# Kernel optimization log

Hardware: AMD Instinct MI355X
Metric: run time of the kernel (lower is better)

Reference implementation:

```python
import jax, jax.numpy as jnp
import numpy as np
import math

B, S, D_VEC, D_HEAD = 4, 4096, 1024, 256


def setup_inputs() -> dict:
    key = jax.random.key(0)
    ks = jax.random.split(key, 10)
    scale = 0.02
    return {
        "x_q": jax.random.normal(ks[0], (B, S, D_VEC), dtype=jnp.float32),
        "x_k": jax.random.normal(ks[1], (B, S, D_VEC), dtype=jnp.float32),
        "x_v": jax.random.normal(ks[2], (B, S, D_VEC), dtype=jnp.float32),
        "mask": jax.random.randint(ks[3], (B, S, S), 0, 2, dtype=jnp.int32),
        "wq_w": jax.random.normal(ks[4], (D_HEAD, D_VEC), dtype=jnp.float32) * scale,
        "wq_b": jnp.zeros((D_HEAD,), dtype=jnp.float32),
        "wk_w": jax.random.normal(ks[5], (D_HEAD, D_VEC), dtype=jnp.float32) * scale,
        "wk_b": jnp.zeros((D_HEAD,), dtype=jnp.float32),
        "wv_w": jax.random.normal(ks[6], (D_HEAD, D_VEC), dtype=jnp.float32) * scale,
        "wv_b": jnp.zeros((D_HEAD,), dtype=jnp.float32),
    }


def reference(x_q, x_k, x_v, mask, wq_w, wq_b, wk_w, wk_b, wv_w, wv_b):
    # Linear projections (torch nn.Linear: x @ W^T + b)
    q = jnp.einsum("bsd,hd->bsh", x_q, wq_w) + wq_b  # [B,S,H]
    k = jnp.einsum("bsd,hd->bsh", x_k, wk_w) + wk_b
    v = jnp.einsum("bsd,hd->bsh", x_v, wv_w) + wv_b
    scores = jnp.einsum("bqh,bkh->bqk", q, k) / math.sqrt(D_HEAD)  # [B,Sq,Sk]
    # NOTE: original uses masked_fill(mask==0, 0) BEFORE softmax (fills with 0, not -inf)
    scores = jnp.where(mask == 0, jnp.zeros((), dtype=scores.dtype), scores)
    attn = jax.nn.softmax(scores, axis=-1)
    return jnp.einsum("bqk,bkh->bqh", attn, v)  # [B,S,H]
```

## Files before the change

kernel.cpp:

```cpp
#include <hip/hip_runtime.h>
#include <cstdint>
#include <cstddef>

#define S_LEN 4096
#define DVEC  1024
#define DH    256

typedef __attribute__((ext_vector_type(8))) short short8;
typedef __attribute__((ext_vector_type(4))) float f32x4;
typedef __attribute__((ext_vector_type(4))) unsigned short ushort4v;

__device__ __forceinline__ unsigned short f2bf(float f) {
  unsigned u = __builtin_bit_cast(unsigned, f);
  u += 0x7FFFu + ((u >> 16) & 1u);
  return (unsigned short)(u >> 16);
}

__device__ __forceinline__ void gl2lds16(const void* g, void* lds) {
  __builtin_amdgcn_global_load_lds(
      (const __attribute__((address_space(1))) unsigned int*)g,
      (__attribute__((address_space(3))) unsigned int*)lds, 16, 0, 0);
}

__global__ void wcvt_kernel(const float* __restrict__ wq,
                            const float* __restrict__ wk,
                            const float* __restrict__ wv,
                            unsigned short* __restrict__ wbf) {
  int t   = blockIdx.x * 256 + threadIdx.x;
  int idx = t * 4;
  int m   = idx >> 18;
  int off = idx & 262143;
  const float* src = (m == 0) ? wq : (m == 1) ? wk : wv;
  float scale = (m == 0) ? 0.0625f : 1.0f;
  f32x4 v = *(const f32x4*)(src + off);
  ushort4v o;
  o.x = f2bf(v.x * scale);
  o.y = f2bf(v.y * scale);
  o.z = f2bf(v.z * scale);
  o.w = f2bf(v.w * scale);
  *(ushort4v*)(wbf + idx) = o;
}

__global__ void proj_kernel(const float* __restrict__ xq,
                            const float* __restrict__ xk,
                            const float* __restrict__ xv,
                            const unsigned short* __restrict__ wbf,
                            const float* __restrict__ bq,
                            const float* __restrict__ bk,
                            const float* __restrict__ bv,
                            unsigned short* __restrict__ qbf,
                            unsigned short* __restrict__ kbf,
                            unsigned short* __restrict__ vtbf) {
  const int tid  = threadIdx.x;
  const int lane = tid & 63;
  const int w    = tid >> 6;
  const int z    = blockIdx.z;
  const int m0   = blockIdx.x * 64;

  const float* x = (z == 0) ? xq : (z == 1) ? xk : xv;
  const unsigned short* wz = wbf + (size_t)z * (DH * DVEC);
  const float* bias = (z == 0) ? bq : (z == 1) ? bk : bv;
  const float bscale = (z == 0) ? 0.0625f : 1.0f;

  __shared__ float At[2][64 * 32];

  f32x4 zero = {0.f, 0.f, 0.f, 0.f};
  f32x4 acc[4][4];
#pragma unroll
  for (int i = 0; i < 4; ++i)
#pragma unroll
    for (int j = 0; j < 4; ++j) acc[i][j] = zero;

  auto stage = [&](int kt, int buf) {
    char* dstb = (char*)&At[buf][0] + w * 2048;
#pragma unroll
    for (int i = 0; i < 2; ++i) {
      int lin  = w * 2048 + i * 1024 + lane * 16;
      int row  = lin >> 7;
      int scol = (lin ^ ((row & 7) << 4)) & 127;
      gl2lds16((const char*)x + ((size_t)(m0 + row) * DVEC + kt * 32) * 4 + scol,
               dstb + i * 1024);
    }
  };

  stage(0, 0);
  __syncthreads();

  for (int kt = 0; kt < 32; ++kt) {
    const int buf = kt & 1;
    if (kt + 1 < 32) stage(kt + 1, buf ^ 1);

    short8 bfr[4];
#pragma unroll
    for (int cf = 0; cf < 4; ++cf) {
      int h = w * 64 + cf * 16 + (lane & 15);
      int d = kt * 32 + (lane >> 4) * 8;
      bfr[cf] = *(const short8*)(wz + (size_t)h * DVEC + d);
    }
    const char* ab = (const char*)&At[buf][0];
#pragma unroll
    for (int rf = 0; rf < 4; ++rf) {
      int row = rf * 16 + (lane & 15);
      int c0  = row * 128 + (lane >> 4) * 32;
      int sw  = (row & 7) << 4;
      f32x4 v0 = *(const f32x4*)(ab + (c0 ^ sw));
      f32x4 v1 = *(const f32x4*)(ab + ((c0 + 16) ^ sw));
      short8 af;
      af[0] = (short)f2bf(v0.x); af[1] = (short)f2bf(v0.y);
      af[2] = (short)f2bf(v0.z); af[3] = (short)f2bf(v0.w);
      af[4] = (short)f2bf(v1.x); af[5] = (short)f2bf(v1.y);
      af[6] = (short)f2bf(v1.z); af[7] = (short)f2bf(v1.w);
#pragma unroll
      for (int cf = 0; cf < 4; ++cf)
        acc[rf][cf] = __builtin_amdgcn_mfma_f32_16x16x32_bf16(af, bfr[cf], acc[rf][cf], 0, 0, 0);
    }
    __syncthreads();
  }

  float bvv[4];
#pragma unroll
  for (int cf = 0; cf < 4; ++cf)
    bvv[cf] = bias[w * 64 + cf * 16 + (lane & 15)] * bscale;

  if (z < 2) {
    unsigned short* o = (z == 0) ? qbf : kbf;
#pragma unroll
    for (int rf = 0; rf < 4; ++rf)
#pragma unroll
      for (int cf = 0; cf < 4; ++cf)
#pragma unroll
        for (int r = 0; r < 4; ++r) {
          int m = m0 + rf * 16 + (lane >> 4) * 4 + r;
          int h = w * 64 + cf * 16 + (lane & 15);
          o[(size_t)m * DH + h] = f2bf(acc[rf][cf][r] + bvv[cf]);
        }
  } else {
    int bb = m0 >> 12;
    int sl = m0 & 4095;
#pragma unroll
    for (int rf = 0; rf < 4; ++rf)
#pragma unroll
      for (int cf = 0; cf < 4; ++cf) {
        int s = sl + rf * 16 + (lane >> 4) * 4;
        int h = w * 64 + cf * 16 + (lane & 15);
        ushort4v o;
        o.x = f2bf(acc[rf][cf][0] + bvv[cf]);
        o.y = f2bf(acc[rf][cf][1] + bvv[cf]);
        o.z = f2bf(acc[rf][cf][2] + bvv[cf]);
        o.w = f2bf(acc[rf][cf][3] + bvv[cf]);
        *(ushort4v*)(vtbf + ((size_t)(bb * DH + h)) * S_LEN + s) = o;
      }
  }
}

__global__ void __launch_bounds__(512, 2)
attn_kernel(const unsigned short* __restrict__ qbf,
            const unsigned short* __restrict__ kbf,
            const unsigned short* __restrict__ vtbf,
            const int* __restrict__ mask,
            float* __restrict__ out) {
  const int tid  = threadIdx.x;
  const int lane = tid & 63;
  const int w    = tid >> 6;
  const int j    = lane & 15;
  const int g    = lane >> 4;

  const int kvs = w & 3;
  const int qh  = w >> 2;
  const int qs  = w >> 2;
  const int hs  = w & 3;

  const int bx = blockIdx.x;
  const int x  = bx & 7;
  const int b  = x >> 1;
  const int qt = (bx >> 3) * 2 + (x & 1);
  const int m0 = qt * 64;

  __shared__ char sbuf[140288];

  short8 qreg[2][8];
#pragma unroll
  for (int qf = 0; qf < 2; ++qf) {
    const unsigned short* qrow =
        qbf + ((size_t)(b * S_LEN + m0 + qh * 32 + qf * 16 + j)) * DH + g * 8;
#pragma unroll
    for (int kc = 0; kc < 8; ++kc) qreg[qf][kc] = *(const short8*)(qrow + kc * 32);
  }

  f32x4 zero = {0.f, 0.f, 0.f, 0.f};
  f32x4 acc[2][4];
#pragma unroll
  for (int a = 0; a < 2; ++a)
#pragma unroll
    for (int hf = 0; hf < 4; ++hf) acc[a][hf] = zero;
  float lrow[2][4] = {{0.f, 0.f, 0.f, 0.f}, {0.f, 0.f, 0.f, 0.f}};

  const int* mb = mask + ((size_t)(b * S_LEN + m0 + qh * 32 + g * 4)) * S_LEN + kvs * 16 + j;

  auto stageK = [&](int t, int buf) {
    const char* src = (const char*)kbf + ((size_t)(b * S_LEN) + t * 64) * 512;
    char* dst = sbuf + buf * 32768 + w * 4096;
#pragma unroll
    for (int i = 0; i < 4; ++i) {
      int rid = w * 4 + i;
      int ks  = rid >> 3;
      int kc  = rid & 7;
      gl2lds16(src + (size_t)(ks * 16 + j) * 512 + kc * 64 + g * 16, dst + i * 1024);
    }
  };
  auto stageV = [&](int t, int buf) {
    char* dst = sbuf + 65536 + buf * 32768 + w * 4096;
#pragma unroll
    for (int i = 0; i < 4; ++i) {
      int rid = w * 4 + i;
      int h16 = rid >> 1;
      int kc2 = rid & 1;
      const char* src = (const char*)vtbf +
          (((size_t)(b * DH + h16 * 16 + j)) * S_LEN + t * 64 + kc2 * 32 + g * 8) * 2;
      gl2lds16(src, dst + i * 1024);
    }
  };

  int mcur[8], mnext[8];
#pragma unroll
  for (int qf = 0; qf < 2; ++qf)
#pragma unroll
    for (int r = 0; r < 4; ++r) mcur[qf * 4 + r] = mb[(qf * 16 + r) * S_LEN];
  stageK(0, 0);
  stageV(0, 0);
  __syncthreads();

  const int pwbase = 131072 + (kvs >> 1) * 1024 + ((kvs & 1) * 2 + (j >> 3)) * 256 + (j & 7) * 2;

  const int NT = S_LEN / 64;
  for (int t = 0; t < NT; ++t) {
    const int buf = t & 1;
    if (t + 1 < NT) {
#pragma unroll
      for (int qf = 0; qf < 2; ++qf)
#pragma unroll
        for (int r = 0; r < 4; ++r)
          mnext[qf * 4 + r] = mb[(qf * 16 + r) * S_LEN + (t + 1) * 64];
      stageK(t + 1, buf ^ 1);
    }

    const char* kb = sbuf + buf * 32768 + kvs * 8192;
    f32x4 s0[2], s1[2];
    s0[0] = zero; s0[1] = zero; s1[0] = zero; s1[1] = zero;
    __builtin_amdgcn_s_setprio(1);
#pragma unroll
    for (int kc = 0; kc < 8; kc += 2) {
      short8 k0 = *(const short8*)(kb + kc * 1024 + lane * 16);
      short8 k1 = *(const short8*)(kb + (kc + 1) * 1024 + lane * 16);
      s0[0] = __builtin_amdgcn_mfma_f32_16x16x32_bf16(qreg[0][kc], k0, s0[0], 0, 0, 0);
      s0[1] = __builtin_amdgcn_mfma_f32_16x16x32_bf16(qreg[1][kc], k0, s0[1], 0, 0, 0);
      s1[0] = __builtin_amdgcn_mfma_f32_16x16x32_bf16(qreg[0][kc + 1], k1, s1[0], 0, 0, 0);
      s1[1] = __builtin_amdgcn_mfma_f32_16x16x32_bf16(qreg[1][kc + 1], k1, s1[1], 0, 0, 0);
    }
    __builtin_amdgcn_s_setprio(0);

#pragma unroll
    for (int qf = 0; qf < 2; ++qf) {
      int cb = pwbase + (qh * 2 + qf) * 2048;
#pragma unroll
      for (int r = 0; r < 4; ++r) {
        float sv = s0[qf][r] + s1[qf][r];
        sv = mcur[qf * 4 + r] ? sv : 0.0f;
        float e = __expf(sv);
        lrow[qf][r] += e;
        *(unsigned short*)(sbuf + cb + (r * 4 + g) * 16) = f2bf(e);
      }
    }
    __syncthreads();

    if (t + 1 < NT) stageV(t + 1, buf ^ 1);

    const char* vb = sbuf + 65536 + buf * 32768 + hs * 8192;
    short8 pf[2][2];
#pragma unroll
    for (int qf2 = 0; qf2 < 2; ++qf2)
#pragma unroll
      for (int kc2 = 0; kc2 < 2; ++kc2)
        pf[qf2][kc2] = *(const short8*)(sbuf + 131072 + ((qs * 2 + qf2) * 2 + kc2) * 1024 + lane * 16);
    __builtin_amdgcn_s_setprio(1);
#pragma unroll
    for (int hf = 0; hf < 4; ++hf) {
      short8 v0 = *(const short8*)(vb + (hf * 2 + 0) * 1024 + lane * 16);
      short8 v1 = *(const short8*)(vb + (hf * 2 + 1) * 1024 + lane * 16);
      acc[0][hf] = __builtin_amdgcn_mfma_f32_16x16x32_bf16(pf[0][0], v0, acc[0][hf], 0, 0, 0);
      acc[1][hf] = __builtin_amdgcn_mfma_f32_16x16x32_bf16(pf[1][0], v0, acc[1][hf], 0, 0, 0);
      acc[0][hf] = __builtin_amdgcn_mfma_f32_16x16x32_bf16(pf[0][1], v1, acc[0][hf], 0, 0, 0);
      acc[1][hf] = __builtin_amdgcn_mfma_f32_16x16x32_bf16(pf[1][1], v1, acc[1][hf], 0, 0, 0);
    }
    __builtin_amdgcn_s_setprio(0);

#pragma unroll
    for (int i = 0; i < 8; ++i) mcur[i] = mnext[i];
    __syncthreads();
  }

#pragma unroll
  for (int qf = 0; qf < 2; ++qf)
#pragma unroll
    for (int r = 0; r < 4; ++r) {
#pragma unroll
      for (int off = 1; off < 16; off <<= 1)
        lrow[qf][r] += __shfl_xor(lrow[qf][r], off, 64);
    }
  float* lbuf = (float*)(sbuf + 139264);
  if (j == 0) {
#pragma unroll
    for (int qf = 0; qf < 2; ++qf)
#pragma unroll
      for (int r = 0; r < 4; ++r)
        lbuf[(qh * 32 + qf * 16 + g * 4 + r) * 4 + kvs] = lrow[qf][r];
  }
  __syncthreads();

#pragma unroll
  for (int qf2 = 0; qf2 < 2; ++qf2)
#pragma unroll
    for (int rr = 0; rr < 4; ++rr) {
      int qb = qs * 32 + qf2 * 16 + rr * 4 + g;
      f32x4 lv = *(const f32x4*)&lbuf[qb * 4];
      float linv = 1.0f / (lv[0] + lv[1] + lv[2] + lv[3]);
      float* orow = out + ((size_t)(b * S_LEN + m0 + qb)) * DH + hs * 64 + j;
#pragma unroll
      for (int hf = 0; hf < 4; ++hf)
        orow[hf * 16] = acc[qf2][hf][rr] * linv;
    }
}

extern "C" void kernel_launch(void* const* d_in, const int* in_sizes, int n_in,
                              void* d_out, int out_size, void* d_ws, size_t ws_size,
                              hipStream_t stream) {
  const float* xq = (const float*)d_in[0];
  const float* xk = (const float*)d_in[1];
  const float* xv = (const float*)d_in[2];
  const int* mask = (const int*)d_in[3];
  const float* wq = (const float*)d_in[4];
  const float* bq = (const float*)d_in[5];
  const float* wk = (const float*)d_in[6];
  const float* bk = (const float*)d_in[7];
  const float* wv = (const float*)d_in[8];
  const float* bv = (const float*)d_in[9];
  float* out = (float*)d_out;

  char* ws = (char*)d_ws;
  unsigned short* wbf  = (unsigned short*)(ws);
  unsigned short* qbf  = (unsigned short*)(ws + (2ull  << 20));
  unsigned short* kbf  = (unsigned short*)(ws + (10ull << 20));
  unsigned short* vtbf = (unsigned short*)(ws + (18ull << 20));

  hipLaunchKernelGGL(wcvt_kernel, dim3(768), dim3(256), 0, stream, wq, wk, wv, wbf);
  hipLaunchKernelGGL(proj_kernel, dim3(256, 1, 3), dim3(256), 0, stream,
                     xq, xk, xv, wbf, bq, bk, bv, qbf, kbf, vtbf);
  hipLaunchKernelGGL(attn_kernel, dim3(256), dim3(512), 0, stream,
                     qbf, kbf, vtbf, mask, out);
}
```

Baseline: 275.3 us.

## Warp-specialize attention: split QK/softmax and PV waves, halve query tile

Restructures the attention kernel so waves 0-3 compute QK^T, masking and exp for a 32-row query tile while waves 4-7 run the PV matmul for the previous KV tile, forming a one-stage software pipeline. V is read straight from global memory instead of being staged through LDS, which cuts LDS use and doubles the grid with a higher occupancy target. The aim is to overlap the softmax/exp phase with the PV MFMAs and raise occupancy. In exchange the K tile is loaded per 32 query rows instead of 64, doubling K traffic, and the V reads from global may expose latency.

```diff
diff --git a/kernel.cpp b/kernel.cpp
--- a/kernel.cpp
+++ b/kernel.cpp
@@ -153,7 +153,7 @@
   }
 }
 
-__global__ void __launch_bounds__(512, 2)
+__global__ void __launch_bounds__(512, 4)
 attn_kernel(const unsigned short* __restrict__ qbf,
             const unsigned short* __restrict__ kbf,
             const unsigned short* __restrict__ vtbf,
@@ -165,41 +165,52 @@
   const int j    = lane & 15;
   const int g    = lane >> 4;
 
-  const int kvs = w & 3;
-  const int qh  = w >> 2;
-  const int qs  = w >> 2;
-  const int hs  = w & 3;
-
   const int bx = blockIdx.x;
   const int x  = bx & 7;
   const int b  = x >> 1;
   const int qt = (bx >> 3) * 2 + (x & 1);
-  const int m0 = qt * 64;
-
-  __shared__ char sbuf[140288];
-
+  const int m0 = qt * 32;
+
+  __shared__ char sbuf[74240];
+  float* lbuf = (float*)(sbuf + 73728);
+
+  const int NT = S_LEN / 64;
+
+  f32x4 zero = {0.f, 0.f, 0.f, 0.f};
+
+  const int kvs = w;
   short8 qreg[2][8];
-#pragma unroll
-  for (int qf = 0; qf < 2; ++qf) {
-    const unsigned short* qrow =
-        qbf + ((size_t)(b * S_LEN + m0 + qh * 32 + qf * 16 + j)) * DH + g * 8;
-#pragma unroll
-    for (int kc = 0; kc < 8; ++kc) qreg[qf][kc] = *(const short8*)(qrow + kc * 32);
-  }
-
-  f32x4 zero = {0.f, 0.f, 0.f, 0.f};
+  float lrow[2][4] = {{0.f,0.f,0.f,0.f},{0.f,0.f,0.f,0.f}};
+  int mcur[8], mnext[8];
+  const int* mb = nullptr;
+  int pjoff = 0;
+  if (w < 4) {
+#pragma unroll
+    for (int qf = 0; qf < 2; ++qf) {
+      const unsigned short* qrow =
+          qbf + ((size_t)(b * S_LEN + m0 + qf * 16 + j)) * DH + g * 8;
+#pragma unroll
+      for (int kc = 0; kc < 8; ++kc) qreg[qf][kc] = *(const short8*)(qrow + kc * 32);
+    }
+    mb = mask + ((size_t)(b * S_LEN + m0 + g * 4)) * S_LEN + kvs * 16 + j;
+    int jj = (kvs & 1) * 16 + j;
+    pjoff = (jj >> 3) * 16 + (jj & 7) * 2;
+#pragma unroll
+    for (int qf = 0; qf < 2; ++qf)
+#pragma unroll
+      for (int r = 0; r < 4; ++r) mcur[qf * 4 + r] = mb[(qf * 16 + r) * S_LEN];
+  }
+
+  const int hs = w - 4;
   f32x4 acc[2][4];
 #pragma unroll
   for (int a = 0; a < 2; ++a)
 #pragma unroll
     for (int hf = 0; hf < 4; ++hf) acc[a][hf] = zero;
-  float lrow[2][4] = {{0.f, 0.f, 0.f, 0.f}, {0.f, 0.f, 0.f, 0.f}};
-
-  const int* mb = mask + ((size_t)(b * S_LEN + m0 + qh * 32 + g * 4)) * S_LEN + kvs * 16 + j;
-
-  auto stageK = [&](int t, int buf) {
-    const char* src = (const char*)kbf + ((size_t)(b * S_LEN) + t * 64) * 512;
-    char* dst = sbuf + buf * 32768 + w * 4096;
+
+  auto stageK = [&](int t1) {
+    const char* src = (const char*)kbf + ((size_t)(b * S_LEN + t1 * 64)) * 512;
+    char* dst = sbuf + (t1 & 1) * 32768 + w * 4096;
 #pragma unroll
     for (int i = 0; i < 4; ++i) {
       int rid = w * 4 + i;
@@ -208,127 +219,112 @@
       gl2lds16(src + (size_t)(ks * 16 + j) * 512 + kc * 64 + g * 16, dst + i * 1024);
     }
   };
-  auto stageV = [&](int t, int buf) {
-    char* dst = sbuf + 65536 + buf * 32768 + w * 4096;
-#pragma unroll
-    for (int i = 0; i < 4; ++i) {
-      int rid = w * 4 + i;
-      int h16 = rid >> 1;
-      int kc2 = rid & 1;
-      const char* src = (const char*)vtbf +
-          (((size_t)(b * DH + h16 * 16 + j)) * S_LEN + t * 64 + kc2 * 32 + g * 8) * 2;
-      gl2lds16(src, dst + i * 1024);
-    }
-  };
-
-  int mcur[8], mnext[8];
-#pragma unroll
-  for (int qf = 0; qf < 2; ++qf)
-#pragma unroll
-    for (int r = 0; r < 4; ++r) mcur[qf * 4 + r] = mb[(qf * 16 + r) * S_LEN];
-  stageK(0, 0);
-  stageV(0, 0);
-  __syncthreads();
-
-  const int pwbase = 131072 + (kvs >> 1) * 1024 + ((kvs & 1) * 2 + (j >> 3)) * 256 + (j & 7) * 2;
-
-  const int NT = S_LEN / 64;
-  for (int t = 0; t < NT; ++t) {
-    const int buf = t & 1;
-    if (t + 1 < NT) {
-#pragma unroll
-      for (int qf = 0; qf < 2; ++qf)
-#pragma unroll
-        for (int r = 0; r < 4; ++r)
-          mnext[qf * 4 + r] = mb[(qf * 16 + r) * S_LEN + (t + 1) * 64];
-      stageK(t + 1, buf ^ 1);
-    }
-
-    const char* kb = sbuf + buf * 32768 + kvs * 8192;
-    f32x4 s0[2], s1[2];
-    s0[0] = zero; s0[1] = zero; s1[0] = zero; s1[1] = zero;
+
+  auto pv = [&](int u) {
+    const char* pb = sbuf + 65536 + (u & 1) * 4096;
+    short8 pf[2][2];
+#pragma unroll
+    for (int qf2 = 0; qf2 < 2; ++qf2)
+#pragma unroll
+      for (int kvc = 0; kvc < 2; ++kvc)
+        pf[qf2][kvc] = *(const short8*)(pb + (qf2 * 2 + kvc) * 1024 + j * 64 + g * 16);
+    const unsigned short* vb =
+        vtbf + ((size_t)(b * DH + hs * 64 + j)) * S_LEN + u * 64 + g * 8;
     __builtin_amdgcn_s_setprio(1);
 #pragma unroll
-    for (int kc = 0; kc < 8; kc += 2) {
-      short8 k0 = *(const short8*)(kb + kc * 1024 + lane * 16);
-      short8 k1 = *(const short8*)(kb + (kc + 1) * 1024 + lane * 16);
-      s0[0] = __builtin_amdgcn_mfma_f32_16x16x32_bf16(qreg[0][kc], k0, s0[0], 0, 0, 0);
-      s0[1] = __builtin_amdgcn_mfma_f32_16x16x32_bf16(qreg[1][kc], k0, s0[1], 0, 0, 0);
-      s1[0] = __builtin_amdgcn_mfma_f32_16x16x32_bf16(qreg[0][kc + 1], k1, s1[0], 0, 0, 0);
-      s1[1] = __builtin_amdgcn_mfma_f32_16x16x32_bf16(qreg[1][kc + 1], k1, s1[1], 0, 0, 0);
-    }
-    __builtin_amdgcn_s_setprio(0);
-
-#pragma unroll
-    for (int qf = 0; qf < 2; ++qf) {
-      int cb = pwbase + (qh * 2 + qf) * 2048;
-#pragma unroll
-      for (int r = 0; r < 4; ++r) {
-        float sv = s0[qf][r] + s1[qf][r];
-        sv = mcur[qf * 4 + r] ? sv : 0.0f;
-        float e = __expf(sv);
-        lrow[qf][r] += e;
-        *(unsigned short*)(sbuf + cb + (r * 4 + g) * 16) = f2bf(e);
-      }
-    }
-    __syncthreads();
-
-    if (t + 1 < NT) stageV(t + 1, buf ^ 1);
-
-    const char* vb = sbuf + 65536 + buf * 32768 + hs * 8192;
-    short8 pf[2][2];
-#pragma unroll
-    for (int qf2 = 0; qf2 < 2; ++qf2)
-#pragma unroll
-      for (int kc2 = 0; kc2 < 2; ++kc2)
-        pf[qf2][kc2] = *(const short8*)(sbuf + 131072 + ((qs * 2 + qf2) * 2 + kc2) * 1024 + lane * 16);
-    __builtin_amdgcn_s_setprio(1);
-#pragma unroll
     for (int hf = 0; hf < 4; ++hf) {
-      short8 v0 = *(const short8*)(vb + (hf * 2 + 0) * 1024 + lane * 16);
-      short8 v1 = *(const short8*)(vb + (hf * 2 + 1) * 1024 + lane * 16);
+      short8 v0 = *(const short8*)(vb + (size_t)(hf * 16) * S_LEN);
+      short8 v1 = *(const short8*)(vb + (size_t)(hf * 16) * S_LEN + 32);
       acc[0][hf] = __builtin_amdgcn_mfma_f32_16x16x32_bf16(pf[0][0], v0, acc[0][hf], 0, 0, 0);
       acc[1][hf] = __builtin_amdgcn_mfma_f32_16x16x32_bf16(pf[1][0], v0, acc[1][hf], 0, 0, 0);
       acc[0][hf] = __builtin_amdgcn_mfma_f32_16x16x32_bf16(pf[0][1], v1, acc[0][hf], 0, 0, 0);
       acc[1][hf] = __builtin_amdgcn_mfma_f32_16x16x32_bf16(pf[1][1], v1, acc[1][hf], 0, 0, 0);
     }
     __builtin_amdgcn_s_setprio(0);
-
-#pragma unroll
-    for (int i = 0; i < 8; ++i) mcur[i] = mnext[i];
+  };
+
+  stageK(0);
+  __syncthreads();
+
+  for (int t = 0; t < NT; ++t) {
+    if (t + 1 < NT) stageK(t + 1);
+
+    if (w < 4) {
+      const char* kb = sbuf + (t & 1) * 32768;
+      f32x4 s0 = zero, s1 = zero;
+      __builtin_amdgcn_s_setprio(1);
+#pragma unroll
+      for (int kc = 0; kc < 8; ++kc) {
+        short8 kf = *(const short8*)(kb + (kvs * 8 + kc) * 1024 + lane * 16);
+        s0 = __builtin_amdgcn_mfma_f32_16x16x32_bf16(qreg[0][kc], kf, s0, 0, 0, 0);
+        s1 = __builtin_amdgcn_mfma_f32_16x16x32_bf16(qreg[1][kc], kf, s1, 0, 0, 0);
+      }
+      __builtin_amdgcn_s_setprio(0);
+
+      if (t + 1 < NT) {
+#pragma unroll
+        for (int qf = 0; qf < 2; ++qf)
+#pragma unroll
+          for (int r = 0; r < 4; ++r)
+            mnext[qf * 4 + r] = mb[(qf * 16 + r) * S_LEN + (t + 1) * 64];
+      }
+
+      char* pb = sbuf + 65536 + (t & 1) * 4096;
+#pragma unroll
+      for (int qf = 0; qf < 2; ++qf) {
+        int sbase = (qf * 2 + (kvs >> 1)) * 1024 + pjoff;
+#pragma unroll
+        for (int r = 0; r < 4; ++r) {
+          float sv = qf ? s1[r] : s0[r];
+          sv = mcur[qf * 4 + r] ? sv : 0.0f;
+          float e = __expf(sv);
+          lrow[qf][r] += e;
+          *(unsigned short*)(pb + sbase + (g * 4 + r) * 64) = f2bf(e);
+        }
+      }
+#pragma unroll
+      for (int i = 0; i < 8; ++i) mcur[i] = mnext[i];
+    } else {
+      if (t > 0) pv(t - 1);
+    }
+
     __syncthreads();
   }
 
-#pragma unroll
-  for (int qf = 0; qf < 2; ++qf)
-#pragma unroll
-    for (int r = 0; r < 4; ++r) {
-#pragma unroll
-      for (int off = 1; off < 16; off <<= 1)
-        lrow[qf][r] += __shfl_xor(lrow[qf][r], off, 64);
-    }
-  float* lbuf = (float*)(sbuf + 139264);
-  if (j == 0) {
+  if (w >= 4) {
+    pv(NT - 1);
+  } else {
 #pragma unroll
     for (int qf = 0; qf < 2; ++qf)
 #pragma unroll
-      for (int r = 0; r < 4; ++r)
-        lbuf[(qh * 32 + qf * 16 + g * 4 + r) * 4 + kvs] = lrow[qf][r];
+      for (int r = 0; r < 4; ++r) {
+#pragma unroll
+        for (int off = 1; off < 16; off <<= 1)
+          lrow[qf][r] += __shfl_xor(lrow[qf][r], off, 64);
+      }
+    if (j == 0) {
+#pragma unroll
+      for (int qf = 0; qf < 2; ++qf)
+#pragma unroll
+        for (int r = 0; r < 4; ++r)
+          lbuf[(qf * 16 + g * 4 + r) * 4 + kvs] = lrow[qf][r];
+    }
   }
   __syncthreads();
 
-#pragma unroll
-  for (int qf2 = 0; qf2 < 2; ++qf2)
-#pragma unroll
-    for (int rr = 0; rr < 4; ++rr) {
-      int qb = qs * 32 + qf2 * 16 + rr * 4 + g;
-      f32x4 lv = *(const f32x4*)&lbuf[qb * 4];
-      float linv = 1.0f / (lv[0] + lv[1] + lv[2] + lv[3]);
-      float* orow = out + ((size_t)(b * S_LEN + m0 + qb)) * DH + hs * 64 + j;
-#pragma unroll
-      for (int hf = 0; hf < 4; ++hf)
-        orow[hf * 16] = acc[qf2][hf][rr] * linv;
-    }
+  if (w >= 4) {
+#pragma unroll
+    for (int qf2 = 0; qf2 < 2; ++qf2)
+#pragma unroll
+      for (int r = 0; r < 4; ++r) {
+        f32x4 lv = *(const f32x4*)&lbuf[(qf2 * 16 + g * 4 + r) * 4];
+        float linv = 1.0f / (lv[0] + lv[1] + lv[2] + lv[3]);
+        float* orow = out + ((size_t)(b * S_LEN + m0 + qf2 * 16 + g * 4 + r)) * DH + hs * 64 + j;
+#pragma unroll
+        for (int hf = 0; hf < 4; ++hf)
+          orow[hf * 16] = acc[qf2][hf][r] * linv;
+      }
+  }
 }
 
 extern "C" void kernel_launch(void* const* d_in, const int* in_sizes, int n_in,
@@ -355,6 +351,6 @@
   hipLaunchKernelGGL(wcvt_kernel, dim3(768), dim3(256), 0, stream, wq, wk, wv, wbf);
   hipLaunchKernelGGL(proj_kernel, dim3(256, 1, 3), dim3(256), 0, stream,
                      xq, xk, xv, wbf, bq, bk, bv, qbf, kbf, vtbf);
-  hipLaunchKernelGGL(attn_kernel, dim3(256), dim3(512), 0, stream,
+  hipLaunchKernelGGL(attn_kernel, dim3(512), dim3(512), 0, stream,
                      qbf, kbf, vtbf, mask, out);
 }
```

New measurement: 442.7 us. 60.8% more time.

## Pack mask into bitmask, load V directly to registers, shrink LDS

Applied to the files above, without the earlier changes.

Adds a pre-pass kernel that compresses the int32 mask into 64-bit ballot words, so the attention kernel reads one bit per element instead of a 4-byte int per score. V tiles are now loaded straight from global memory into registers instead of being staged through LDS. This halves the shared-memory footprint and raises the launch bound to 4 waves-per-EU hint. The cost is an extra full pass over the 256MB mask, plus uncoalesced-ish direct V loads. The attention grid of 256 blocks still gives at most one block per CU, so the extra occupancy may go unused.

```diff
diff --git a/kernel.cpp b/kernel.cpp
--- a/kernel.cpp
+++ b/kernel.cpp
@@ -9,6 +9,7 @@
 typedef __attribute__((ext_vector_type(8))) short short8;
 typedef __attribute__((ext_vector_type(4))) float f32x4;
 typedef __attribute__((ext_vector_type(4))) unsigned short ushort4v;
+typedef unsigned long long ull;
 
 __device__ __forceinline__ unsigned short f2bf(float f) {
   unsigned u = __builtin_bit_cast(unsigned, f);
@@ -20,6 +21,31 @@
   __builtin_amdgcn_global_load_lds(
       (const __attribute__((address_space(1))) unsigned int*)g,
       (__attribute__((address_space(3))) unsigned int*)lds, 16, 0, 0);
+}
+
+__global__ void mcomp_kernel(const int* __restrict__ mask,
+                             ull* __restrict__ mbits) {
+  const int lane = threadIdx.x & 63;
+  const int wid  = (int)((blockIdx.x * blockDim.x + threadIdx.x) >> 6);
+  const size_t base = (size_t)wid * 256;
+#pragma unroll 4
+  for (int i = 0; i < 64; ++i) {
+    size_t w0 = base + (size_t)i * 4;
+    int v0 = mask[(w0 + 0) * 64 + lane];
+    int v1 = mask[(w0 + 1) * 64 + lane];
+    int v2 = mask[(w0 + 2) * 64 + lane];
+    int v3 = mask[(w0 + 3) * 64 + lane];
+    ull b0 = __ballot(v0 != 0);
+    ull b1 = __ballot(v1 != 0);
+    ull b2 = __ballot(v2 != 0);
+    ull b3 = __ballot(v3 != 0);
+    if (lane == 0) {
+      mbits[w0 + 0] = b0;
+      mbits[w0 + 1] = b1;
+      mbits[w0 + 2] = b2;
+      mbits[w0 + 3] = b3;
+    }
+  }
 }
 
 __global__ void wcvt_kernel(const float* __restrict__ wq,
@@ -153,11 +179,11 @@
   }
 }
 
-__global__ void __launch_bounds__(512, 2)
+__global__ void __launch_bounds__(512, 4)
 attn_kernel(const unsigned short* __restrict__ qbf,
             const unsigned short* __restrict__ kbf,
             const unsigned short* __restrict__ vtbf,
-            const int* __restrict__ mask,
+            const ull* __restrict__ mbits,
             float* __restrict__ out) {
   const int tid  = threadIdx.x;
   const int lane = tid & 63;
@@ -176,7 +202,8 @@
   const int qt = (bx >> 3) * 2 + (x & 1);
   const int m0 = qt * 64;
 
-  __shared__ char sbuf[140288];
+  __shared__ char sbuf[74752];
+  float* lbuf = (float*)(sbuf + 73728);
 
   short8 qreg[2][8];
 #pragma unroll
@@ -193,13 +220,16 @@
   for (int a = 0; a < 2; ++a)
 #pragma unroll
     for (int hf = 0; hf < 4; ++hf) acc[a][hf] = zero;
-  float lrow[2][4] = {{0.f, 0.f, 0.f, 0.f}, {0.f, 0.f, 0.f, 0.f}};
-
-  const int* mb = mask + ((size_t)(b * S_LEN + m0 + qh * 32 + g * 4)) * S_LEN + kvs * 16 + j;
-
-  auto stageK = [&](int t, int buf) {
-    const char* src = (const char*)kbf + ((size_t)(b * S_LEN) + t * 64) * 512;
-    char* dst = sbuf + buf * 32768 + w * 4096;
+  float lrow[2][4] = {{0.f,0.f,0.f,0.f},{0.f,0.f,0.f,0.f}};
+  short8 vreg[4][2];
+
+  const ull* mwb = mbits + ((size_t)(b * S_LEN + m0 + qh * 32 + g * 4)) * 64;
+  const int mbit = kvs * 16 + j;
+  int mcur[8], mnext[8];
+
+  auto stageK = [&](int t1, int bufbase) {
+    const char* src = (const char*)kbf + ((size_t)(b * S_LEN + t1 * 64)) * 512;
+    char* dst = sbuf + bufbase + w * 4096;
 #pragma unroll
     for (int i = 0; i < 4; ++i) {
       int rid = w * 4 + i;
@@ -208,40 +238,39 @@
       gl2lds16(src + (size_t)(ks * 16 + j) * 512 + kc * 64 + g * 16, dst + i * 1024);
     }
   };
-  auto stageV = [&](int t, int buf) {
-    char* dst = sbuf + 65536 + buf * 32768 + w * 4096;
-#pragma unroll
-    for (int i = 0; i < 4; ++i) {
-      int rid = w * 4 + i;
-      int h16 = rid >> 1;
-      int kc2 = rid & 1;
-      const char* src = (const char*)vtbf +
-          (((size_t)(b * DH + h16 * 16 + j)) * S_LEN + t * 64 + kc2 * 32 + g * 8) * 2;
-      gl2lds16(src, dst + i * 1024);
-    }
-  };
-
-  int mcur[8], mnext[8];
+
+  const unsigned short* vbase =
+      vtbf + ((size_t)(b * DH + hs * 64 + j)) * S_LEN;
+
+  const int pwbase = 65536 + (kvs >> 1) * 1024 + ((kvs & 1) * 2 + (j >> 3)) * 256 + (j & 7) * 2;
+
+  stageK(0, 0);
 #pragma unroll
   for (int qf = 0; qf < 2; ++qf)
 #pragma unroll
-    for (int r = 0; r < 4; ++r) mcur[qf * 4 + r] = mb[(qf * 16 + r) * S_LEN];
-  stageK(0, 0);
-  stageV(0, 0);
+    for (int r = 0; r < 4; ++r)
+      mcur[qf * 4 + r] = (int)((mwb[(qf * 16 + r) * 64] >> mbit) & 1ull);
   __syncthreads();
-
-  const int pwbase = 131072 + (kvs >> 1) * 1024 + ((kvs & 1) * 2 + (j >> 3)) * 256 + (j & 7) * 2;
 
   const int NT = S_LEN / 64;
   for (int t = 0; t < NT; ++t) {
     const int buf = t & 1;
     if (t + 1 < NT) {
+      stageK(t + 1, (buf ^ 1) * 32768);
 #pragma unroll
       for (int qf = 0; qf < 2; ++qf)
 #pragma unroll
         for (int r = 0; r < 4; ++r)
-          mnext[qf * 4 + r] = mb[(qf * 16 + r) * S_LEN + (t + 1) * 64];
-      stageK(t + 1, buf ^ 1);
+          mnext[qf * 4 + r] = (int)((mwb[(qf * 16 + r) * 64 + t + 1] >> mbit) & 1ull);
+    }
+
+    {
+      const unsigned short* vt = vbase + t * 64 + g * 8;
+#pragma unroll
+      for (int hf = 0; hf < 4; ++hf)
+#pragma unroll
+        for (int kvc = 0; kvc < 2; ++kvc)
+          vreg[hf][kvc] = *(const short8*)(vt + (size_t)(hf * 16) * S_LEN + kvc * 32);
     }
 
     const char* kb = sbuf + buf * 32768 + kvs * 8192;
@@ -273,24 +302,19 @@
     }
     __syncthreads();
 
-    if (t + 1 < NT) stageV(t + 1, buf ^ 1);
-
-    const char* vb = sbuf + 65536 + buf * 32768 + hs * 8192;
     short8 pf[2][2];
 #pragma unroll
     for (int qf2 = 0; qf2 < 2; ++qf2)
 #pragma unroll
-      for (int kc2 = 0; kc2 < 2; ++kc2)
-        pf[qf2][kc2] = *(const short8*)(sbuf + 131072 + ((qs * 2 + qf2) * 2 + kc2) * 1024 + lane * 16);
+      for (int kvc = 0; kvc < 2; ++kvc)
+        pf[qf2][kvc] = *(const short8*)(sbuf + 65536 + ((qs * 2 + qf2) * 2 + kvc) * 1024 + lane * 16);
     __builtin_amdgcn_s_setprio(1);
 #pragma unroll
     for (int hf = 0; hf < 4; ++hf) {
-      short8 v0 = *(const short8*)(vb + (hf * 2 + 0) * 1024 + lane * 16);
-      short8 v1 = *(const short8*)(vb + (hf * 2 + 1) * 1024 + lane * 16);
-      acc[0][hf] = __builtin_amdgcn_mfma_f32_16x16x32_bf16(pf[0][0], v0, acc[0][hf], 0, 0, 0);
-      acc[1][hf] = __builtin_amdgcn_mfma_f32_16x16x32_bf16(pf[1][0], v0, acc[1][hf], 0, 0, 0);
-      acc[0][hf] = __builtin_amdgcn_mfma_f32_16x16x32_bf16(pf[0][1], v1, acc[0][hf], 0, 0, 0);
-      acc[1][hf] = __builtin_amdgcn_mfma_f32_16x16x32_bf16(pf[1][1], v1, acc[1][hf], 0, 0, 0);
+      acc[0][hf] = __builtin_amdgcn_mfma_f32_16x16x32_bf16(pf[0][0], vreg[hf][0], acc[0][hf], 0, 0, 0);
+      acc[1][hf] = __builtin_amdgcn_mfma_f32_16x16x32_bf16(pf[1][0], vreg[hf][0], acc[1][hf], 0, 0, 0);
+      acc[0][hf] = __builtin_amdgcn_mfma_f32_16x16x32_bf16(pf[0][1], vreg[hf][1], acc[0][hf], 0, 0, 0);
+      acc[1][hf] = __builtin_amdgcn_mfma_f32_16x16x32_bf16(pf[1][1], vreg[hf][1], acc[1][hf], 0, 0, 0);
     }
     __builtin_amdgcn_s_setprio(0);
 
@@ -307,7 +331,6 @@
       for (int off = 1; off < 16; off <<= 1)
         lrow[qf][r] += __shfl_xor(lrow[qf][r], off, 64);
     }
-  float* lbuf = (float*)(sbuf + 139264);
   if (j == 0) {
 #pragma unroll
     for (int qf = 0; qf < 2; ++qf)
@@ -351,10 +374,12 @@
   unsigned short* qbf  = (unsigned short*)(ws + (2ull  << 20));
   unsigned short* kbf  = (unsigned short*)(ws + (10ull << 20));
   unsigned short* vtbf = (unsigned short*)(ws + (18ull << 20));
-
+  ull*            mbit = (ull*)           (ws + (26ull << 20));
+
+  hipLaunchKernelGGL(mcomp_kernel, dim3(1024), dim3(256), 0, stream, mask, mbit);
   hipLaunchKernelGGL(wcvt_kernel, dim3(768), dim3(256), 0, stream, wq, wk, wv, wbf);
   hipLaunchKernelGGL(proj_kernel, dim3(256, 1, 3), dim3(256), 0, stream,
                      xq, xk, xv, wbf, bq, bk, bv, qbf, kbf, vtbf);
   hipLaunchKernelGGL(attn_kernel, dim3(256), dim3(512), 0, stream,
-                     qbf, kbf, vtbf, mask, out);
-}
+                     qbf, kbf, vtbf, mbit, out);
+}
```

New measurement: 763.1 us. 2.77x slower.

## Precompress int32 mask into bitmasks with ballot before attention

Applied to the files above, without the earlier changes.

Adds a pre-pass kernel that reads the int32 mask with coalesced loads and packs each 64-key chunk into a 64-bit word using wave ballots. The attention kernel then reads one 64-bit word per row per tile and extracts its bit, instead of issuing scattered 4-byte mask loads inside the main loop. This aims to take mask bandwidth and latency off the attention kernel's critical loop. The cost is an extra launch that still streams the full mask once, plus a small bitmask write and read. The pre-pass keeps only a few loads in flight per wave, so it could limit how fully memory bandwidth is used.

```diff
diff --git a/kernel.cpp b/kernel.cpp
--- a/kernel.cpp
+++ b/kernel.cpp
@@ -9,6 +9,7 @@
 typedef __attribute__((ext_vector_type(8))) short short8;
 typedef __attribute__((ext_vector_type(4))) float f32x4;
 typedef __attribute__((ext_vector_type(4))) unsigned short ushort4v;
+typedef unsigned long long ull;
 
 __device__ __forceinline__ unsigned short f2bf(float f) {
   unsigned u = __builtin_bit_cast(unsigned, f);
@@ -20,6 +21,31 @@
   __builtin_amdgcn_global_load_lds(
       (const __attribute__((address_space(1))) unsigned int*)g,
       (__attribute__((address_space(3))) unsigned int*)lds, 16, 0, 0);
+}
+
+__global__ void mcomp_kernel(const int* __restrict__ mask,
+                             ull* __restrict__ mbits) {
+  const int lane = threadIdx.x & 63;
+  const int wid  = (int)((blockIdx.x * blockDim.x + threadIdx.x) >> 6);
+  const size_t base = (size_t)wid * 256;
+#pragma unroll 4
+  for (int i = 0; i < 64; ++i) {
+    size_t w0 = base + (size_t)i * 4;
+    int v0 = mask[(w0 + 0) * 64 + lane];
+    int v1 = mask[(w0 + 1) * 64 + lane];
+    int v2 = mask[(w0 + 2) * 64 + lane];
+    int v3 = mask[(w0 + 3) * 64 + lane];
+    ull b0 = __ballot(v0 != 0);
+    ull b1 = __ballot(v1 != 0);
+    ull b2 = __ballot(v2 != 0);
+    ull b3 = __ballot(v3 != 0);
+    if (lane == 0) {
+      mbits[w0 + 0] = b0;
+      mbits[w0 + 1] = b1;
+      mbits[w0 + 2] = b2;
+      mbits[w0 + 3] = b3;
+    }
+  }
 }
 
 __global__ void wcvt_kernel(const float* __restrict__ wq,
@@ -157,7 +183,7 @@
 attn_kernel(const unsigned short* __restrict__ qbf,
             const unsigned short* __restrict__ kbf,
             const unsigned short* __restrict__ vtbf,
-            const int* __restrict__ mask,
+            const ull* __restrict__ mbits,
             float* __restrict__ out) {
   const int tid  = threadIdx.x;
   const int lane = tid & 63;
@@ -195,7 +221,8 @@
     for (int hf = 0; hf < 4; ++hf) acc[a][hf] = zero;
   float lrow[2][4] = {{0.f, 0.f, 0.f, 0.f}, {0.f, 0.f, 0.f, 0.f}};
 
-  const int* mb = mask + ((size_t)(b * S_LEN + m0 + qh * 32 + g * 4)) * S_LEN + kvs * 16 + j;
+  const ull* mwb = mbits + ((size_t)(b * S_LEN + m0 + qh * 32 + g * 4)) * 64;
+  const int mbit = kvs * 16 + j;
 
   auto stageK = [&](int t, int buf) {
     const char* src = (const char*)kbf + ((size_t)(b * S_LEN) + t * 64) * 512;
@@ -225,7 +252,8 @@
 #pragma unroll
   for (int qf = 0; qf < 2; ++qf)
 #pragma unroll
-    for (int r = 0; r < 4; ++r) mcur[qf * 4 + r] = mb[(qf * 16 + r) * S_LEN];
+    for (int r = 0; r < 4; ++r)
+      mcur[qf * 4 + r] = (int)((mwb[(qf * 16 + r) * 64] >> mbit) & 1ull);
   stageK(0, 0);
   stageV(0, 0);
   __syncthreads();
@@ -240,7 +268,7 @@
       for (int qf = 0; qf < 2; ++qf)
 #pragma unroll
         for (int r = 0; r < 4; ++r)
-          mnext[qf * 4 + r] = mb[(qf * 16 + r) * S_LEN + (t + 1) * 64];
+          mnext[qf * 4 + r] = (int)((mwb[(qf * 16 + r) * 64 + t + 1] >> mbit) & 1ull);
       stageK(t + 1, buf ^ 1);
     }
 
@@ -351,10 +379,12 @@
   unsigned short* qbf  = (unsigned short*)(ws + (2ull  << 20));
   unsigned short* kbf  = (unsigned short*)(ws + (10ull << 20));
   unsigned short* vtbf = (unsigned short*)(ws + (18ull << 20));
-
+  ull*            mbit = (ull*)           (ws + (26ull << 20));
+
+  hipLaunchKernelGGL(mcomp_kernel, dim3(1024), dim3(256), 0, stream, mask, mbit);
   hipLaunchKernelGGL(wcvt_kernel, dim3(768), dim3(256), 0, stream, wq, wk, wv, wbf);
   hipLaunchKernelGGL(proj_kernel, dim3(256, 1, 3), dim3(256), 0, stream,
                      xq, xk, xv, wbf, bq, bk, bv, qbf, kbf, vtbf);
   hipLaunchKernelGGL(attn_kernel, dim3(256), dim3(512), 0, stream,
-                     qbf, kbf, vtbf, mask, out);
-}
+                     qbf, kbf, vtbf, mbit, out);
+}
```

Measured after the change: 355.2 us. +29.0%, slower.
